# Kernel optimization log

Measured on AMD Instinct MI355X. Metric: run time of the kernel, lower is better.

The kernel has to match this reference:

```python
import jax, jax.numpy as jnp
import numpy as np

D_MODEL = 1024
NUM_HEADS = 16
DEPTH = D_MODEL // NUM_HEADS


def setup_inputs() -> dict:
    key = jax.random.key(0)
    ks = jax.random.split(key, 11)
    B, S = 4, 2048
    scale = 1.0 / np.sqrt(D_MODEL)
    inp = {
        "q": jax.random.normal(ks[0], (B, S, D_MODEL), jnp.float32),
        "k": jax.random.normal(ks[1], (B, S, D_MODEL), jnp.float32),
        "v": jax.random.normal(ks[2], (B, S, D_MODEL), jnp.float32),
        # Linear params (weight stored [out, in] like torch; applied as x @ W.T + b)
        "wq_w": jax.random.normal(ks[3], (D_MODEL, D_MODEL), jnp.float32) * scale,
        "wq_b": jnp.zeros((D_MODEL,), jnp.float32),
        "wk_w": jax.random.normal(ks[4], (D_MODEL, D_MODEL), jnp.float32) * scale,
        "wk_b": jnp.zeros((D_MODEL,), jnp.float32),
        "wv_w": jax.random.normal(ks[5], (D_MODEL, D_MODEL), jnp.float32) * scale,
        "wv_b": jnp.zeros((D_MODEL,), jnp.float32),
        "wo_w": jax.random.normal(ks[6], (D_MODEL, D_MODEL), jnp.float32) * scale,
        "wo_b": jnp.zeros((D_MODEL,), jnp.float32),
    }
    return inp


def _split_heads(x, B, S):
    # [B, S, D] -> [B, H, S, depth]
    return x.reshape(B, S, NUM_HEADS, DEPTH).transpose(0, 2, 1, 3)


def reference(q, k, v, wq_w, wq_b, wk_w, wk_b, wv_w, wv_b, wo_w, wo_b):
    B, S, _ = q.shape
    qh = _split_heads(q @ wq_w.T + wq_b, B, S)
    kh = _split_heads(k @ wk_w.T + wk_b, B, S)
    vh = _split_heads(v @ wv_w.T + wv_b, B, S)
    # scaled dot-product attention: [B, H, Sq, Sk]
    scores = jnp.einsum("bhqd,bhkd->bhqk", qh, kh) / jnp.sqrt(
        jnp.asarray(DEPTH, qh.dtype))
    attn = jax.nn.softmax(scores, axis=-1)
    ctx = jnp.einsum("bhqk,bhkd->bhqd", attn, vh)
    # [B, H, S, depth] -> [B, S, D]
    ctx = ctx.transpose(0, 2, 1, 3).reshape(B, S, D_MODEL)
    return ctx @ wo_w.T + wo_b
```

## Files before the change

kernel.cpp:

```cpp
#include <hip/hip_runtime.h>
#include <hip/hip_bf16.h>

typedef __attribute__((ext_vector_type(8))) short bf16x8;
typedef __attribute__((ext_vector_type(4))) short bf16x4;
typedef __attribute__((ext_vector_type(4))) float f32x4;
typedef __attribute__((address_space(3))) ushort lds_ushort;

#define MFMA32(a, b, c) __builtin_amdgcn_mfma_f32_16x16x32_bf16(a, b, c, 0, 0, 0)
#if __has_builtin(__builtin_amdgcn_mfma_f32_16x16x16bf16_1k)
#define HAVE_MFMA16K 1
#define MFMA16K(a, b, c) __builtin_amdgcn_mfma_f32_16x16x16bf16_1k(a, b, c, 0, 0, 0)
#else
#define HAVE_MFMA16K 0
#endif

#define ASYNC16(g, l)                                                          \
    __builtin_amdgcn_global_load_lds(                                          \
        (const __attribute__((address_space(1))) unsigned int*)(g),            \
        (__attribute__((address_space(3))) unsigned int*)(l), 16, 0, 0)

#define TR16(dst, addr, OFF)                                                   \
    asm volatile("ds_read_b64_tr_b16 %0, %1 offset:%2"                         \
                 : "=v"(dst) : "v"(addr), "i"(OFF))

__device__ __forceinline__ ushort f2bf(float f) {
    __hip_bfloat16 h = __float2bfloat16(f);
    return *reinterpret_cast<ushort*>(&h);
}
__device__ __forceinline__ uint cvtpk(float a, float b) {
    uint r;
    asm("v_cvt_pk_bf16_f32 %0, %1, %2" : "=v"(r) : "v"(a), "v"(b));
    return r;
}

#define QSCALE 0.18033688011112042f

struct CvtArgs { const float* s[7]; ushort* d[7]; int nb[7]; };

__global__ __launch_bounds__(256) void cvtk(CvtArgs a) {
    const int z = blockIdx.y;
    if ((int)blockIdx.x >= a.nb[z]) return;
    const float* s = a.s[z];
    ushort* d = a.d[z];
    const size_t i = (size_t)blockIdx.x * 2048 + threadIdx.x * 8;
    float4 f0 = *(const float4*)&s[i];
    float4 f1 = *(const float4*)&s[i + 4];
    *(ushort4*)&d[i]     = make_ushort4(f2bf(f0.x), f2bf(f0.y), f2bf(f0.z), f2bf(f0.w));
    *(ushort4*)&d[i + 4] = make_ushort4(f2bf(f1.x), f2bf(f1.y), f2bf(f1.z), f2bf(f1.w));
}

struct GemmArgs {
    const ushort* X[3]; const ushort* W[3]; const float* B[3];
    void* O[3]; int mode[3]; float scale[3];
};

__global__ __launch_bounds__(512, 4) void gemmk(GemmArgs g) {
    extern __shared__ __attribute__((aligned(16))) ushort smem[];

    const int z = blockIdx.z;
    const ushort* __restrict__ X = g.X[z];
    const ushort* __restrict__ W = g.W[z];
    const float*  __restrict__ bias = g.B[z];
    const int mode = g.mode[z];
    const float scale = g.scale[z];

    const int tid  = threadIdx.x;
    const int lane = tid & 63;
    const int wave = tid >> 6;
    const int quad = (lane >> 4) & 3;
    const int l16  = lane & 15;
    const int wm   = (wave >> 2) * 64;
    const int wn   = (wave & 3) * 32;

    const int flat = blockIdx.x + 8 * blockIdx.y;
    const int t0   = (flat & 7) * 64 + (flat >> 3);
    const int m0   = (t0 >> 3) * 128;
    const int n0   = (t0 & 7) * 128;

    f32x4 acc[4][2];
#pragma unroll
    for (int i = 0; i < 4; i++)
#pragma unroll
        for (int j = 0; j < 2; j++) acc[i][j] = (f32x4)0.0f;

    auto issue = [&](int s) {
        if (s >= 64) return;
        const int tile = s >> 2;
        const int buf  = tile & 1;
        const int kind = s & 3;
        const int k0   = tile * 64;
        const int row  = tid >> 3;
        const int gp   = (tid & 7) ^ (row & 7);
        if (kind < 2) {
            ASYNC16(&W[(size_t)(n0 + kind * 64 + row) * 1024 + k0 + gp * 8],
                    smem + 16384 + buf * 8192 + kind * 4096 + wave * 512);
        } else {
            const int half = kind - 2;
            ASYNC16(&X[(size_t)(m0 + half * 64 + row) * 1024 + k0 + gp * 8],
                    smem + buf * 8192 + half * 4096 + wave * 512);
        }
    };

    for (int s = 0; s < 6; s++) issue(s);
    asm volatile("s_waitcnt vmcnt(2)" ::: "memory");
    __builtin_amdgcn_sched_barrier(0);
    __builtin_amdgcn_s_barrier();

    const int sw = l16 & 7;

    for (int t = 0; t < 16; t++) {
        const ushort* A  = smem + (t & 1) * 8192;
        const ushort* Bm = smem + 16384 + (t & 1) * 8192;
        bf16x8 bfrag[2][2];
#pragma unroll
        for (int p = 0; p < 4; p++) {
            issue(4 * t + p + 6);
            if (p == 0) {
#pragma unroll
                for (int nj = 0; nj < 2; nj++)
#pragma unroll
                    for (int ks = 0; ks < 2; ks++) {
                        const int br = wn + nj * 16 + l16;
                        bfrag[nj][ks] = *(const bf16x8*)
                            &Bm[(size_t)(br >> 6) * 4096 + (br & 63) * 64
                                + (((ks * 4 + quad) ^ sw) * 8)];
                    }
            }
            bf16x8 af[2];
#pragma unroll
            for (int ks = 0; ks < 2; ks++) {
                const int ar = wm + p * 16 + l16;
                af[ks] = *(const bf16x8*)
                    &A[(size_t)(ar >> 6) * 4096 + (ar & 63) * 64
                       + (((ks * 4 + quad) ^ sw) * 8)];
            }
            __builtin_amdgcn_s_barrier();
            asm volatile("s_waitcnt lgkmcnt(0)" ::: "memory");
            __builtin_amdgcn_sched_barrier(0);
            __builtin_amdgcn_s_setprio(1);
#pragma unroll
            for (int nj = 0; nj < 2; nj++) {
                acc[p][nj] = MFMA32(af[0], bfrag[nj][0], acc[p][nj]);
                acc[p][nj] = MFMA32(af[1], bfrag[nj][1], acc[p][nj]);
            }
            __builtin_amdgcn_s_setprio(0);
            if (p == 3) {
                if (t < 14) {
                    asm volatile("s_waitcnt vmcnt(2)" ::: "memory");
                } else {
                    asm volatile("s_waitcnt vmcnt(0)" ::: "memory");
                }
                __builtin_amdgcn_sched_barrier(0);
            }
            __builtin_amdgcn_s_barrier();
        }
    }

#pragma unroll
    for (int mi = 0; mi < 4; mi++) {
#pragma unroll
        for (int nj = 0; nj < 2; nj++) {
            const int n  = n0 + wn + nj * 16 + l16;
            const float bb = bias[n];
#pragma unroll
            for (int r = 0; r < 4; r++) {
                const int m = m0 + wm + mi * 16 + quad * 4 + r;
                const float val = (acc[mi][nj][r] + bb) * scale;
                if (mode == 2) {
                    ((float*)g.O[z])[(size_t)m * 1024 + n] = val;
                } else {
                    const int bat = m >> 11, s = m & 2047, h = n >> 6, d = n & 63;
                    ((ushort*)g.O[z])[((size_t)((bat * 16 + h) * 2048 + s)) * 64 + d]
                        = f2bf(val);
                }
            }
        }
    }
}

__global__ __launch_bounds__(256, 4) void attn(
    const ushort* __restrict__ Qp, const ushort* __restrict__ Kp,
    const ushort* __restrict__ Vp, ushort* __restrict__ ctx)
{
    __shared__ __attribute__((aligned(16))) ushort Ks[2][2 * 64 * 32];
    __shared__ __attribute__((aligned(16))) ushort Vs[2][64 * 64];

    const int tid  = threadIdx.x;
    const int lane = tid & 63;
    const int wave = tid >> 6;
    const int quad = lane >> 4;
    const int l16  = lane & 15;

    const int id = blockIdx.x;
    const int bh = (id & 7) * 8 + ((id >> 3) & 7);
    const int q0 = (id >> 6) * 128;
    const int b  = bh >> 4, h = bh & 15;

    const ushort* Qg = Qp + ((size_t)bh * 2048 + q0) * 64;
    const ushort* Kg = Kp + (size_t)bh * 2048 * 64;
    const ushort* Vg = Vp + (size_t)bh * 2048 * 64;

    bf16x8 aq[2][2];
#pragma unroll
    for (int st = 0; st < 2; st++)
#pragma unroll
        for (int kk = 0; kk < 2; kk++)
            aq[st][kk] = *(const bf16x8*)&Qg[(size_t)(wave * 32 + st * 16 + l16) * 64
                                            + kk * 32 + quad * 8];

    f32x4 o[2][4];
#pragma unroll
    for (int st = 0; st < 2; st++)
#pragma unroll
        for (int jd = 0; jd < 4; jd++) o[st][jd] = (f32x4)0.0f;
#if HAVE_MFMA16K
    f32x4 ls[2] = {(f32x4)0.0f, (f32x4)0.0f};
    union { uint u[2]; bf16x4 v; } ones;
    ones.u[0] = 0x3F803F80u; ones.u[1] = 0x3F803F80u;
#else
    float lsum[2] = {0.f, 0.f};
#endif

    auto stage = [&](int buf, int n0) {
#pragma unroll
        for (int j = 0; j < 2; j++) {
            const int c    = j * 256 + tid;
            const int colq = c & 3;
            const int row  = (c >> 2) & 63;
            const int half = c >> 8;
            ASYNC16(&Kg[(size_t)(n0 + row) * 64 + half * 32 + colq * 8],
                    &Ks[buf][0] + (size_t)(j * 256 + wave * 64) * 8);
        }
#pragma unroll
        for (int j = 0; j < 2; j++) {
            const int c   = j * 256 + tid;
            const int key = ((c >> 5) << 2) | ((c >> 1) & 3);
            const int d   = (((c >> 3) & 3) << 4) | ((c & 1) << 3);
            ASYNC16(&Vg[(size_t)(n0 + key) * 64 + d],
                    &Vs[buf][0] + (size_t)(j * 256 + wave * 64) * 8);
        }
    };

    stage(0, 0);
    int cur = 0;

    for (int n0 = 0; n0 < 2048; n0 += 64) {
        __syncthreads();
        if (n0 + 64 < 2048) stage(cur ^ 1, n0 + 64);

        uint pk[4][2][2];
#pragma unroll
        for (int kb = 0; kb < 4; kb++) {
            bf16x8 kf0 = *(const bf16x8*)&Ks[cur][(size_t)(kb * 16 + l16) * 32 + quad * 8];
            bf16x8 kf1 = *(const bf16x8*)&Ks[cur][(size_t)(64 + kb * 16 + l16) * 32 + quad * 8];
#pragma unroll
            for (int st = 0; st < 2; st++) {
                f32x4 s = (f32x4)0.0f;
                s = MFMA32(kf0, aq[st][0], s);
                s = MFMA32(kf1, aq[st][1], s);
                float e0 = __builtin_amdgcn_exp2f(s[0]);
                float e1 = __builtin_amdgcn_exp2f(s[1]);
                float e2 = __builtin_amdgcn_exp2f(s[2]);
                float e3 = __builtin_amdgcn_exp2f(s[3]);
                pk[kb][st][0] = cvtpk(e0, e1);
                pk[kb][st][1] = cvtpk(e2, e3);
#if !HAVE_MFMA16K
                lsum[st] += (e0 + e1) + (e2 + e3);
#endif
            }
        }

#if HAVE_MFMA16K
        const lds_ushort* vp = (const lds_ushort*)&Vs[cur][0] + quad * 256 + l16 * 4;
        bf16x4 vf[4][4];
#define TRISSUE(JD)                                                            \
        TR16(vf[JD][0], vp, (JD) * 128 + 0);                                   \
        TR16(vf[JD][1], vp, (JD) * 128 + 2048);                                \
        TR16(vf[JD][2], vp, (JD) * 128 + 4096);                                \
        TR16(vf[JD][3], vp, (JD) * 128 + 6144);
        TRISSUE(0) TRISSUE(1) TRISSUE(2) TRISSUE(3)

#pragma unroll
        for (int kb = 0; kb < 4; kb++) {
#pragma unroll
            for (int st = 0; st < 2; st++) {
                union { uint u[2]; bf16x4 v; } pf;
                pf.u[0] = pk[kb][st][0];
                pf.u[1] = pk[kb][st][1];
                ls[st] = MFMA16K(pf.v, ones.v, ls[st]);
            }
        }

#define PVWAIT(N)                                                              \
        asm volatile("s_waitcnt lgkmcnt(" #N ")" ::: "memory");                \
        __builtin_amdgcn_sched_barrier(0);
#define PVJD(JD)                                                               \
        _Pragma("unroll")                                                      \
        for (int kb = 0; kb < 4; kb++) {                                       \
            _Pragma("unroll")                                                  \
            for (int st = 0; st < 2; st++) {                                   \
                union { uint u[2]; bf16x4 v; } pf;                             \
                pf.u[0] = pk[kb][st][0];                                       \
                pf.u[1] = pk[kb][st][1];                                       \
                o[st][JD] = MFMA16K(pf.v, vf[JD][kb], o[st][JD]);              \
            }                                                                  \
        }
        __builtin_amdgcn_s_setprio(1);
        PVWAIT(12) PVJD(0)
        PVWAIT(8)  PVJD(1)
        PVWAIT(4)  PVJD(2)
        PVWAIT(0)  PVJD(3)
        __builtin_amdgcn_s_setprio(0);
#else
        const int addr0 = 4 * ((2 * (quad & 1)) * 16 + l16);
        const int addr1 = addr0 + 64;
#pragma unroll
        for (int kt = 0; kt < 2; kt++) {
            bf16x8 apf[2];
#pragma unroll
            for (int st = 0; st < 2; st++) {
                union { uint u[4]; bf16x8 v; } t;
#pragma unroll
                for (int j = 0; j < 4; j++) {
                    uint src = (quad & 2) ? pk[kt * 2 + 1][st][j & 1]
                                          : pk[kt * 2][st][j & 1];
                    t.u[j] = (uint)__builtin_amdgcn_ds_bpermute(
                        (j >> 1) ? addr1 : addr0, (int)src);
                }
                apf[st] = t.v;
            }
#pragma unroll
            for (int jd = 0; jd < 4; jd++) {
                union { ushort s[8]; bf16x8 v; } vv;
#pragma unroll
                for (int e = 0; e < 8; e++) {
                    const int key = kt * 32 + quad * 8 + e;
                    const int d   = jd * 16 + l16;
                    vv.s[e] = Vs[cur][(key >> 2) * 256 + (d >> 4) * 64
                                      + (key & 3) * 16 + (d & 15)];
                }
#pragma unroll
                for (int st = 0; st < 2; st++)
                    o[st][jd] = MFMA32(apf[st], vv.v, o[st][jd]);
            }
        }
#endif
        cur ^= 1;
    }

#if HAVE_MFMA16K
#pragma unroll
    for (int st = 0; st < 2; st++) {
        float inv[4];
#pragma unroll
        for (int r = 0; r < 4; r++) inv[r] = 1.0f / ls[st][r];
#pragma unroll
        for (int jd = 0; jd < 4; jd++) {
#pragma unroll
            for (int r = 0; r < 4; r++) {
                const int s = q0 + wave * 32 + st * 16 + quad * 4 + r;
                ctx[((size_t)(b * 2048 + s)) * 1024 + h * 64 + jd * 16 + l16] =
                    f2bf(o[st][jd][r] * inv[r]);
            }
        }
    }
#else
#pragma unroll
    for (int st = 0; st < 2; st++) {
        float lsv = lsum[st];
        lsv += __shfl_xor(lsv, 16, 64);
        lsv += __shfl_xor(lsv, 32, 64);
        float inv[4];
#pragma unroll
        for (int r = 0; r < 4; r++)
            inv[r] = 1.0f / __shfl(lsv, quad * 4 + r, 64);
#pragma unroll
        for (int jd = 0; jd < 4; jd++) {
#pragma unroll
            for (int r = 0; r < 4; r++) {
                const int s = q0 + wave * 32 + st * 16 + quad * 4 + r;
                ctx[((size_t)(b * 2048 + s)) * 1024 + h * 64 + jd * 16 + l16] =
                    f2bf(o[st][jd][r] * inv[r]);
            }
        }
    }
#endif
}

extern "C" void kernel_launch(void* const* d_in, const int* in_sizes, int n_in,
                              void* d_out, int out_size, void* d_ws, size_t ws_size,
                              hipStream_t stream) {
    const float* q    = (const float*)d_in[0];
    const float* k    = (const float*)d_in[1];
    const float* v    = (const float*)d_in[2];
    const float* wq_w = (const float*)d_in[3];
    const float* wq_b = (const float*)d_in[4];
    const float* wk_w = (const float*)d_in[5];
    const float* wk_b = (const float*)d_in[6];
    const float* wv_w = (const float*)d_in[7];
    const float* wv_b = (const float*)d_in[8];
    const float* wo_w = (const float*)d_in[9];
    const float* wo_b = (const float*)d_in[10];
    float* out = (float*)d_out;

    const size_t NE = (size_t)4 * 2048 * 1024;
    const size_t NW = (size_t)1024 * 1024;
    const size_t need_fused = (6 * NE + 4 * NW) * 2;
    const size_t LDSB = 65536;

    dim3 blk(256);
    dim3 gblk(512);
    dim3 ggrid(8, 64, 3);
    dim3 ggrid1(8, 64, 1);

    if (ws_size >= need_fused) {
        ushort* Xq = (ushort*)d_ws;
        ushort* Xk = Xq + NE;
        ushort* Xv = Xk + NE;
        ushort* Wq = Xv + NE;
        ushort* Wk = Wq + NW;
        ushort* Wv = Wk + NW;
        ushort* Wo = Wv + NW;
        ushort* Qp = Wo + NW;
        ushort* Kp = Qp + NE;
        ushort* Vp = Kp + NE;
        ushort* ctx = Xq;

        CvtArgs ca;
        ca.s[0]=q;    ca.d[0]=Xq; ca.nb[0]=4096;
        ca.s[1]=k;    ca.d[1]=Xk; ca.nb[1]=4096;
        ca.s[2]=v;    ca.d[2]=Xv; ca.nb[2]=4096;
        ca.s[3]=wq_w; ca.d[3]=Wq; ca.nb[3]=512;
        ca.s[4]=wk_w; ca.d[4]=Wk; ca.nb[4]=512;
        ca.s[5]=wv_w; ca.d[5]=Wv; ca.nb[5]=512;
        ca.s[6]=wo_w; ca.d[6]=Wo; ca.nb[6]=512;
        cvtk<<<dim3(4096, 7), blk, 0, stream>>>(ca);

        GemmArgs ga;
        ga.X[0]=Xq; ga.W[0]=Wq; ga.B[0]=wq_b; ga.O[0]=Qp; ga.mode[0]=0; ga.scale[0]=QSCALE;
        ga.X[1]=Xk; ga.W[1]=Wk; ga.B[1]=wk_b; ga.O[1]=Kp; ga.mode[1]=0; ga.scale[1]=1.0f;
        ga.X[2]=Xv; ga.W[2]=Wv; ga.B[2]=wv_b; ga.O[2]=Vp; ga.mode[2]=0; ga.scale[2]=1.0f;
        gemmk<<<ggrid, gblk, LDSB, stream>>>(ga);

        attn<<<dim3(1024), blk, 0, stream>>>(Qp, Kp, Vp, ctx);

        GemmArgs go;
        for (int i = 0; i < 3; i++) {
            go.X[i]=ctx; go.W[i]=Wo; go.B[i]=wo_b;
            go.O[i]=out; go.mode[i]=2; go.scale[i]=1.0f;
        }
        gemmk<<<ggrid1, gblk, LDSB, stream>>>(go);
    } else {
        ushort* Xb  = (ushort*)d_ws;
        ushort* Wb  = Xb + NE;
        ushort* Wob = Wb + NW;
        ushort* Qp  = Wob + NW;
        ushort* Kp  = Qp + NE;
        ushort* Vp  = Kp + NE;
        ushort* ctx = Xb;

        const float* xs[3] = {q, k, v};
        const float* ws[3] = {wq_w, wk_w, wv_w};
        const float* bs[3] = {wq_b, wk_b, wv_b};
        ushort* os[3] = {Qp, Kp, Vp};
        for (int p = 0; p < 3; p++) {
            CvtArgs c;
            c.s[0]=xs[p]; c.d[0]=Xb; c.nb[0]=4096;
            c.s[1]=ws[p]; c.d[1]=Wb; c.nb[1]=512;
            for (int i = 2; i < 7; i++) { c.s[i]=xs[p]; c.d[i]=Xb; c.nb[i]=0; }
            cvtk<<<dim3(4096, 2), blk, 0, stream>>>(c);
            GemmArgs gg;
            for (int i = 0; i < 3; i++) {
                gg.X[i]=Xb; gg.W[i]=Wb; gg.B[i]=bs[p]; gg.O[i]=os[p];
                gg.mode[i]=0; gg.scale[i]=(p == 0) ? QSCALE : 1.0f;
            }
            gemmk<<<ggrid1, gblk, LDSB, stream>>>(gg);
        }

        attn<<<dim3(1024), blk, 0, stream>>>(Qp, Kp, Vp, ctx);

        CvtArgs c;
        c.s[0]=wo_w; c.d[0]=Wob; c.nb[0]=512;
        for (int i = 1; i < 7; i++) { c.s[i]=wo_w; c.d[i]=Wob; c.nb[i]=0; }
        cvtk<<<dim3(512, 1), blk, 0, stream>>>(c);
        GemmArgs go;
        for (int i = 0; i < 3; i++) {
            go.X[i]=ctx; go.W[i]=Wob; go.B[i]=wo_b;
            go.O[i]=out; go.mode[i]=2; go.scale[i]=1.0f;
        }
        gemmk<<<ggrid1, gblk, LDSB, stream>>>(go);
    }
}
```

Before: 326.2 us.

## Triple-buffer weight tiles and batch per-tile loads in projection GEMM

Restructures the projection GEMM's software pipeline. The weight (B) tile moves to a three-stage LDS ring and is prefetched two tiles ahead, while the activation tile stays double-buffered one tile ahead. Each k-tile's async loads are now issued together, and the four per-subtile barrier phases collapse into a single phase that loads all A fragments and runs all MFMAs. This cuts barrier count and raises prefetch depth, but LDS per block grows to 80KB, which can lower occupancy and adds register pressure from holding eight A fragments.

```diff
diff --git a/kernel.cpp b/kernel.cpp
--- a/kernel.cpp
+++ b/kernel.cpp
@@ -83,25 +83,36 @@
 #pragma unroll
         for (int j = 0; j < 2; j++) acc[i][j] = (f32x4)0.0f;
 
-    auto issue = [&](int s) {
-        if (s >= 64) return;
-        const int tile = s >> 2;
-        const int buf  = tile & 1;
-        const int kind = s & 3;
-        const int k0   = tile * 64;
-        const int row  = tid >> 3;
-        const int gp   = (tid & 7) ^ (row & 7);
-        if (kind < 2) {
-            ASYNC16(&W[(size_t)(n0 + kind * 64 + row) * 1024 + k0 + gp * 8],
-                    smem + 16384 + buf * 8192 + kind * 4096 + wave * 512);
-        } else {
-            const int half = kind - 2;
-            ASYNC16(&X[(size_t)(m0 + half * 64 + row) * 1024 + k0 + gp * 8],
-                    smem + buf * 8192 + half * 4096 + wave * 512);
+    auto issueA = [&](int tile) {
+        if (tile >= 16) return;
+        const int k0 = tile * 64;
+        ushort* dst = smem + (tile & 1) * 8192;
+#pragma unroll
+        for (int j = 0; j < 2; j++) {
+            const int c   = j * 512 + tid;
+            const int row = c >> 3;
+            const int gp  = (c & 7) ^ (row & 7);
+            ASYNC16(&X[(size_t)(m0 + row) * 1024 + k0 + gp * 8],
+                    dst + (size_t)(j * 512 + wave * 64) * 8);
         }
     };
-
-    for (int s = 0; s < 6; s++) issue(s);
+    auto issueB = [&](int tile) {
+        if (tile >= 16) return;
+        const int k0 = tile * 64;
+        ushort* dst = smem + 16384 + (tile % 3) * 8192;
+#pragma unroll
+        for (int j = 0; j < 2; j++) {
+            const int c   = j * 512 + tid;
+            const int row = c >> 3;
+            const int gp  = (c & 7) ^ (row & 7);
+            ASYNC16(&W[(size_t)(n0 + row) * 1024 + k0 + gp * 8],
+                    dst + (size_t)(j * 512 + wave * 64) * 8);
+        }
+    };
+
+    issueB(0);
+    issueA(0);
+    issueB(1);
     asm volatile("s_waitcnt vmcnt(2)" ::: "memory");
     __builtin_amdgcn_sched_barrier(0);
     __builtin_amdgcn_s_barrier();
@@ -110,50 +121,49 @@
 
     for (int t = 0; t < 16; t++) {
         const ushort* A  = smem + (t & 1) * 8192;
-        const ushort* Bm = smem + 16384 + (t & 1) * 8192;
+        const ushort* Bm = smem + 16384 + (t % 3) * 8192;
+
+        issueA(t + 1);
+        issueB(t + 2);
+
         bf16x8 bfrag[2][2];
 #pragma unroll
-        for (int p = 0; p < 4; p++) {
-            issue(4 * t + p + 6);
-            if (p == 0) {
-#pragma unroll
-                for (int nj = 0; nj < 2; nj++)
-#pragma unroll
-                    for (int ks = 0; ks < 2; ks++) {
-                        const int br = wn + nj * 16 + l16;
-                        bfrag[nj][ks] = *(const bf16x8*)
-                            &Bm[(size_t)(br >> 6) * 4096 + (br & 63) * 64
-                                + (((ks * 4 + quad) ^ sw) * 8)];
-                    }
-            }
-            bf16x8 af[2];
+        for (int nj = 0; nj < 2; nj++)
 #pragma unroll
             for (int ks = 0; ks < 2; ks++) {
-                const int ar = wm + p * 16 + l16;
-                af[ks] = *(const bf16x8*)
-                    &A[(size_t)(ar >> 6) * 4096 + (ar & 63) * 64
-                       + (((ks * 4 + quad) ^ sw) * 8)];
-            }
-            __builtin_amdgcn_s_barrier();
-            asm volatile("s_waitcnt lgkmcnt(0)" ::: "memory");
-            __builtin_amdgcn_sched_barrier(0);
-            __builtin_amdgcn_s_setprio(1);
+                const int br = wn + nj * 16 + l16;
+                bfrag[nj][ks] = *(const bf16x8*)
+                    &Bm[(size_t)br * 64 + (((ks * 4 + quad) ^ sw) * 8)];
+            }
+        bf16x8 af[4][2];
+#pragma unroll
+        for (int i = 0; i < 4; i++)
+#pragma unroll
+            for (int ks = 0; ks < 2; ks++) {
+                const int ar = wm + i * 16 + l16;
+                af[i][ks] = *(const bf16x8*)
+                    &A[(size_t)ar * 64 + (((ks * 4 + quad) ^ sw) * 8)];
+            }
+
+        __builtin_amdgcn_s_barrier();
+        asm volatile("s_waitcnt lgkmcnt(0)" ::: "memory");
+        __builtin_amdgcn_sched_barrier(0);
+        __builtin_amdgcn_s_setprio(1);
+#pragma unroll
+        for (int i = 0; i < 4; i++)
 #pragma unroll
             for (int nj = 0; nj < 2; nj++) {
-                acc[p][nj] = MFMA32(af[0], bfrag[nj][0], acc[p][nj]);
-                acc[p][nj] = MFMA32(af[1], bfrag[nj][1], acc[p][nj]);
-            }
-            __builtin_amdgcn_s_setprio(0);
-            if (p == 3) {
-                if (t < 14) {
-                    asm volatile("s_waitcnt vmcnt(2)" ::: "memory");
-                } else {
-                    asm volatile("s_waitcnt vmcnt(0)" ::: "memory");
-                }
-                __builtin_amdgcn_sched_barrier(0);
-            }
-            __builtin_amdgcn_s_barrier();
-        }
+                acc[i][nj] = MFMA32(af[i][0], bfrag[nj][0], acc[i][nj]);
+                acc[i][nj] = MFMA32(af[i][1], bfrag[nj][1], acc[i][nj]);
+            }
+        __builtin_amdgcn_s_setprio(0);
+        if (t < 14) {
+            asm volatile("s_waitcnt vmcnt(2)" ::: "memory");
+        } else {
+            asm volatile("s_waitcnt vmcnt(0)" ::: "memory");
+        }
+        __builtin_amdgcn_sched_barrier(0);
+        __builtin_amdgcn_s_barrier();
     }
 
 #pragma unroll
@@ -406,7 +416,7 @@
     const size_t NE = (size_t)4 * 2048 * 1024;
     const size_t NW = (size_t)1024 * 1024;
     const size_t need_fused = (6 * NE + 4 * NW) * 2;
-    const size_t LDSB = 65536;
+    const size_t LDSB = 81920;
 
     dim3 blk(256);
     dim3 gblk(512);
```

New measurement: 329.6 us. No clear change (+1.0%).
